# Optimization experiments

Measured on AMD Instinct MI355X. Metric: run time of the kernel, lower is better.

Reference implementation:

```python
import math
import jax, jax.numpy as jnp
import numpy as np
from jax import lax

INPUT_SIZE = 736
PATCH_SIZE = 16
PATCH_LENGTH = 768
EMBED_DIM = 768
BATCH = 32
N_RINGS = INPUT_SIZE // 2  # 368 rings, equal_interval=1


def _precompute_gather(input_size=INPUT_SIZE, patch_length=PATCH_LENGTH):
    """Replicates the torch buffer construction: per-radius-ring pixel masks
    sorted by angle, fused with the per-ring linear (align_corners=True)
    resize to patch_length. Returns flat gather indices and lerp weights."""
    H = W = input_size
    yc = np.arange(H) - (H - 1) / 2.0
    xc = np.arange(W) - (W - 1) / 2.0
    yy, xx = np.meshgrid(yc, xc, indexing='ij')  # yy=row offset, xx=col offset
    radius = np.sqrt(xx ** 2 + yy ** 2)
    R = input_size // 2
    off = (W - 1) / 2.0
    j = np.arange(patch_length)
    idx0_all, idx1_all, w_all = [], [], []
    for low in range(R):
        high = low + 1
        m = (radius > low) & (radius <= high)
        ry, rx = np.nonzero(m)  # row-major order, same as torch .nonzero()
        # Faithful to torch quirk: unbind names (x, y) = (row-off, col-off)
        xv = ry - off
        yv = rx - off
        deg = np.arctan2(-yv, xv) * 180.0 / math.pi
        flat = ry * W + rx
        order = np.argsort(deg, kind='stable')
        flat = flat[order]
        L = len(flat)
        # F.interpolate(mode='linear', align_corners=True) to patch_length
        if L == 1:
            src = np.zeros(patch_length)
        else:
            src = j * (L - 1) / (patch_length - 1)
        i0 = np.clip(np.floor(src).astype(np.int64), 0, L - 1)
        i1 = np.minimum(i0 + 1, L - 1)
        wt = (src - i0).astype(np.float32)
        idx0_all.append(flat[i0])
        idx1_all.append(flat[i1])
        w_all.append(wt)
    idx0 = np.concatenate(idx0_all).astype(np.int32)
    idx1 = np.concatenate(idx1_all).astype(np.int32)
    w = np.concatenate(w_all).astype(np.float32)
    return idx0, idx1, w


def setup_inputs() -> dict:
    key = jax.random.key(0)
    k1, k2 = jax.random.split(key)
    x = jax.random.normal(k1, (BATCH, 3, INPUT_SIZE, INPUT_SIZE), dtype=jnp.float32)
    fan_in = 3 * PATCH_SIZE * PATCH_SIZE
    conv_w = jax.random.normal(k2, (EMBED_DIM, 3, PATCH_SIZE, PATCH_SIZE), dtype=jnp.float32) / np.sqrt(fan_in)
    conv_b = jnp.zeros((EMBED_DIM,), dtype=jnp.float32)
    idx0, idx1, w = _precompute_gather()
    return {
        'x': x,
        'conv_w': conv_w,
        'conv_b': conv_b,
        'idx0': jnp.asarray(idx0),
        'idx1': jnp.asarray(idx1),
        'w': jnp.asarray(w),
    }


def reference(x, conv_w, conv_b, idx0, idx1, w):
    N = x.shape[0]
    flat = x.reshape(N, 3, -1)  # [N, 3, H*W]
    # Fused irregular gather + per-ring linear resize (lerp between neighbors)
    g0 = flat[:, :, idx0]
    g1 = flat[:, :, idx1]
    patches = g0 * (1.0 - w) + g1 * w  # [N, 3, N_RINGS*PATCH_LENGTH]
    patches = patches.reshape(N, 3, N_RINGS, PATCH_LENGTH)  # [N,3,368,768]
    out = lax.conv_general_dilated(
        patches, conv_w,
        window_strides=(PATCH_SIZE, PATCH_SIZE),
        padding='VALID',
        dimension_numbers=('NCHW', 'OIHW', 'NCHW'),
    )
    return out + conv_b[None, :, None, None]  # [N, 768, 23, 48]
```

## Files before the change

kernel.cpp:

```cpp
#include <hip/hip_runtime.h>
#include <hip/hip_bf16.h>
#include <stdint.h>

#define INPUT_SIZE   736
#define PLANE_ELEMS  (736*736)
#define N_RINGS      368
#define PATCH_LEN    768
#define EMBED        768
#define BATCH        32
#define KDIM         768
#define M_TOTAL      (BATCH*23*48)
#define P_PER_BATCH  1104
#define OUT_BATCH_STRIDE 847872
#define GATHER_T     (N_RINGS*PATCH_LEN)

typedef __bf16 bf16x8 __attribute__((ext_vector_type(8)));
typedef float  floatx4 __attribute__((ext_vector_type(4)));

static __device__ __forceinline__ unsigned short bf16bits(float f) {
    __hip_bfloat16 h = __float2bfloat16(f);
    return *reinterpret_cast<unsigned short*>(&h);
}

__global__ void wcast_kernel(const float* __restrict__ wsrc,
                             __hip_bfloat16* __restrict__ Wb) {
    int i = blockIdx.x * 256 + threadIdx.x;
    Wb[i] = __float2bfloat16(wsrc[i]);
}

__global__ void pack_kernel(const int*   __restrict__ idx0,
                            const int*   __restrict__ idx1,
                            const float* __restrict__ w,
                            int2* __restrict__ P) {
    int t = blockIdx.x * 256 + threadIdx.x;
    int i0 = idx0[t];
    int d  = idx1[t] - i0;
    unsigned w16 = (unsigned)(w[t] * 65536.0f);
    if (w16 > 65535u) w16 = 65535u;
    P[t] = make_int2(i0, (int)((w16 << 16) | ((unsigned)d & 0xFFFFu)));
}

__global__ void gather_kernel(const float* __restrict__ x,
                              const int2*  __restrict__ P,
                              __hip_bfloat16* __restrict__ A) {
    int b    = blockIdx.x;
    int half = b & 1;
    int bb   = b >> 1;
    int band = bb % 23;
    int nc   = bb / 23;
    int c    = nc % 3;
    int n    = nc / 3;
    const float* plane = x + (size_t)nc * PLANE_ELEMS;

    int wv   = threadIdx.x >> 6;
    int lane = threadIdx.x & 63;
    int rr   = lane >> 2;
    int ps   = lane & 3;
    int aw   = wv >> 1;
    int hb   = wv & 1;
    int r    = band * 16 + rr;

    int tbase = r * PATCH_LEN + half * 384 + aw * 16 + hb * 8 + ps * 2;
    int k     = c * 256 + rr * 16 + hb * 8 + ps * 2;
    size_t mbase = (size_t)(n * P_PER_BATCH + band * 48 + half * 24 + aw);
    __hip_bfloat16* aptr = A + mbase * KDIM + k;

    #pragma unroll 4
    for (int it = 0; it < 12; it++) {
        int4 q = *reinterpret_cast<const int4*>(&P[tbase + it * 32]);
        int   i0a = q.x;
        int   i1a = i0a + (int)(short)((unsigned)q.y & 0xFFFFu);
        float wa  = (float)((unsigned)q.y >> 16) * (1.0f / 65536.0f);
        float va  = plane[i0a] * (1.0f - wa) + plane[i1a] * wa;
        int   i0b = q.z;
        int   i1b = i0b + (int)(short)((unsigned)q.w & 0xFFFFu);
        float wb  = (float)((unsigned)q.w >> 16) * (1.0f / 65536.0f);
        float vb  = plane[i0b] * (1.0f - wb) + plane[i1b] * wb;
        *reinterpret_cast<ushort2*>(aptr + (size_t)(it * 2) * KDIM) =
            make_ushort2(bf16bits(va), bf16bits(vb));
    }
}

__global__ __launch_bounds__(256) void gemm_kernel(
        const __hip_bfloat16* __restrict__ A,
        const __hip_bfloat16* __restrict__ Wb,
        const float* __restrict__ cb,
        float* __restrict__ out)
{
    __shared__ __hip_bfloat16 As[128 * 32];
    __shared__ __hip_bfloat16 Bs[128 * 32];

    const int tid  = threadIdx.x;
    const int lane = tid & 63;
    const int wv   = tid >> 6;
    const int wm   = wv & 1;
    const int wn   = wv >> 1;
    const int quad = lane >> 4;
    const int l16  = lane & 15;

    const int bn = blockIdx.x;
    const int bm = blockIdx.y;

    floatx4 acc[4][4];
    #pragma unroll
    for (int i = 0; i < 4; i++)
        #pragma unroll
        for (int j = 0; j < 4; j++)
            acc[i][j] = (floatx4){0.f, 0.f, 0.f, 0.f};

    const int srow = tid >> 2;
    const int kofs = (tid & 3) * 8;
    const __hip_bfloat16* aSrc = A  + (size_t)(bm * 128 + srow) * KDIM + kofs;
    const __hip_bfloat16* bSrc = Wb + (size_t)(bn * 128 + srow) * KDIM + kofs;
    __hip_bfloat16* aDst = As + tid * 8;
    __hip_bfloat16* bDst = Bs + tid * 8;

    for (int kt = 0; kt < 24; kt++) {
        const __hip_bfloat16* ap = aSrc + kt * 32;
        const __hip_bfloat16* bp = bSrc + kt * 32;
        __builtin_amdgcn_global_load_lds(
            (const __attribute__((address_space(1))) void*)(const void*)ap,
            (__attribute__((address_space(3))) void*)(void*)aDst, 16, 0, 0);
        __builtin_amdgcn_global_load_lds(
            (const __attribute__((address_space(1))) void*)(const void*)(ap + (size_t)64 * KDIM),
            (__attribute__((address_space(3))) void*)(void*)(aDst + 64 * 32), 16, 0, 0);
        __builtin_amdgcn_global_load_lds(
            (const __attribute__((address_space(1))) void*)(const void*)bp,
            (__attribute__((address_space(3))) void*)(void*)bDst, 16, 0, 0);
        __builtin_amdgcn_global_load_lds(
            (const __attribute__((address_space(1))) void*)(const void*)(bp + (size_t)64 * KDIM),
            (__attribute__((address_space(3))) void*)(void*)(bDst + 64 * 32), 16, 0, 0);
        __syncthreads();

        bf16x8 af[4], bfr[4];
        #pragma unroll
        for (int mi = 0; mi < 4; mi++) {
            int ml = wm * 64 + mi * 16 + l16;
            af[mi] = *(const bf16x8*)(As + ml * 32 + quad * 8);
        }
        #pragma unroll
        for (int ni = 0; ni < 4; ni++) {
            int el = wn * 64 + ni * 16 + l16;
            bfr[ni] = *(const bf16x8*)(Bs + el * 32 + quad * 8);
        }
        #pragma unroll
        for (int mi = 0; mi < 4; mi++)
            #pragma unroll
            for (int ni = 0; ni < 4; ni++)
                acc[mi][ni] = __builtin_amdgcn_mfma_f32_16x16x32_bf16(
                                  af[mi], bfr[ni], acc[mi][ni], 0, 0, 0);
        __syncthreads();
    }

    const int m0 = bm * 128 + wm * 64;
    const int e0 = bn * 128 + wn * 64;
    #pragma unroll
    for (int ni = 0; ni < 4; ni++) {
        int eg = e0 + ni * 16 + l16;
        float bias = cb[eg];
        #pragma unroll
        for (int mi = 0; mi < 4; mi++) {
            int mg = m0 + mi * 16 + quad * 4;
            int nb = mg / P_PER_BATCH;
            int p  = mg - nb * P_PER_BATCH;
            floatx4 v = acc[mi][ni];
            v[0] += bias; v[1] += bias; v[2] += bias; v[3] += bias;
            *(floatx4*)(out + (size_t)nb * OUT_BATCH_STRIDE
                            + (size_t)eg * P_PER_BATCH + p) = v;
        }
    }
}

extern "C" void kernel_launch(void* const* d_in, const int* in_sizes, int n_in,
                              void* d_out, int out_size, void* d_ws, size_t ws_size,
                              hipStream_t stream) {
    const float* x      = (const float*)d_in[0];
    const float* conv_w = (const float*)d_in[1];
    const float* conv_b = (const float*)d_in[2];
    const int*   idx0   = (const int*)  d_in[3];
    const int*   idx1   = (const int*)  d_in[4];
    const float* w      = (const float*)d_in[5];
    float* out = (float*)d_out;

    __hip_bfloat16* A  = (__hip_bfloat16*)d_ws;
    __hip_bfloat16* Wb = A + (size_t)M_TOTAL * KDIM;
    int2*           P  = (int2*)(Wb + (size_t)EMBED * KDIM);

    wcast_kernel<<<dim3(EMBED * KDIM / 256), dim3(256), 0, stream>>>(conv_w, Wb);

    pack_kernel<<<dim3(GATHER_T / 256), dim3(256), 0, stream>>>(idx0, idx1, w, P);

    gather_kernel<<<dim3(BATCH * 3 * (N_RINGS / 16) * 2), dim3(256), 0, stream>>>(
        x, P, A);

    gemm_kernel<<<dim3(EMBED / 128, M_TOTAL / 128), dim3(256), 0, stream>>>(
        A, Wb, conv_b, out);
}
```

Before: 440.7 us.

## Rewrite GEMM with 256x128 tiles, multi-stage LDS pipeline and swizzled layout

Result: slower. 450.3 us (+2.2%).

```diff
diff --git a/kernel.cpp b/kernel.cpp
--- a/kernel.cpp
+++ b/kernel.cpp
@@ -21,6 +21,12 @@
     __hip_bfloat16 h = __float2bfloat16(f);
     return *reinterpret_cast<unsigned short*>(&h);
 }
+
+#define GLDS(gptr, lptr) __builtin_amdgcn_global_load_lds( \
+    (const __attribute__((address_space(1))) void*)(const void*)(gptr), \
+    (__attribute__((address_space(3))) void*)(void*)(lptr), 16, 0, 0)
+#define FENCE() asm volatile("" ::: "memory")
+#define BAR()   do { FENCE(); __builtin_amdgcn_s_barrier(); FENCE(); } while (0)
 
 __global__ void wcast_kernel(const float* __restrict__ wsrc,
                              __hip_bfloat16* __restrict__ Wb) {
@@ -81,20 +87,20 @@
     }
 }
 
-__global__ __launch_bounds__(256) void gemm_kernel(
-        const __hip_bfloat16* __restrict__ A,
+__global__ __launch_bounds__(512) void gemm_kernel(
+        const __hip_bfloat16* __restrict__ Ap,
         const __hip_bfloat16* __restrict__ Wb,
         const float* __restrict__ cb,
         float* __restrict__ out)
 {
-    __shared__ __hip_bfloat16 As[128 * 32];
-    __shared__ __hip_bfloat16 Bs[128 * 32];
+    __shared__ __hip_bfloat16 As[3 * 256 * 64];
+    __shared__ __hip_bfloat16 Bs[2 * 128 * 64];
 
     const int tid  = threadIdx.x;
     const int lane = tid & 63;
     const int wv   = tid >> 6;
-    const int wm   = wv & 1;
-    const int wn   = wv >> 1;
+    const int wm   = wv >> 1;
+    const int wn   = wv & 1;
     const int quad = lane >> 4;
     const int l16  = lane & 15;
 
@@ -108,51 +114,110 @@
         for (int j = 0; j < 4; j++)
             acc[i][j] = (floatx4){0.f, 0.f, 0.f, 0.f};
 
-    const int srow = tid >> 2;
-    const int kofs = (tid & 3) * 8;
-    const __hip_bfloat16* aSrc = A  + (size_t)(bm * 128 + srow) * KDIM + kofs;
-    const __hip_bfloat16* bSrc = Wb + (size_t)(bn * 128 + srow) * KDIM + kofs;
-    __hip_bfloat16* aDst = As + tid * 8;
-    __hip_bfloat16* bDst = Bs + tid * 8;
-
-    for (int kt = 0; kt < 24; kt++) {
-        const __hip_bfloat16* ap = aSrc + kt * 32;
-        const __hip_bfloat16* bp = bSrc + kt * 32;
-        __builtin_amdgcn_global_load_lds(
-            (const __attribute__((address_space(1))) void*)(const void*)ap,
-            (__attribute__((address_space(3))) void*)(void*)aDst, 16, 0, 0);
-        __builtin_amdgcn_global_load_lds(
-            (const __attribute__((address_space(1))) void*)(const void*)(ap + (size_t)64 * KDIM),
-            (__attribute__((address_space(3))) void*)(void*)(aDst + 64 * 32), 16, 0, 0);
-        __builtin_amdgcn_global_load_lds(
-            (const __attribute__((address_space(1))) void*)(const void*)bp,
-            (__attribute__((address_space(3))) void*)(void*)bDst, 16, 0, 0);
-        __builtin_amdgcn_global_load_lds(
-            (const __attribute__((address_space(1))) void*)(const void*)(bp + (size_t)64 * KDIM),
-            (__attribute__((address_space(3))) void*)(void*)(bDst + 64 * 32), 16, 0, 0);
-        __syncthreads();
-
-        bf16x8 af[4], bfr[4];
-        #pragma unroll
-        for (int mi = 0; mi < 4; mi++) {
-            int ml = wm * 64 + mi * 16 + l16;
-            af[mi] = *(const bf16x8*)(As + ml * 32 + quad * 8);
+    const __hip_bfloat16* aG[4]; __hip_bfloat16* aL[4];
+    #pragma unroll
+    for (int l = 0; l < 4; l++) {
+        int u   = l * 512 + tid;
+        int row = u >> 3;
+        int col = ((u & 7) ^ (row & 7)) * 8;
+        aG[l] = Ap + (size_t)(bm * 256 + row) * KDIM + col;
+        aL[l] = As + u * 8;
+    }
+    const __hip_bfloat16* bG[2]; __hip_bfloat16* bL[2];
+    #pragma unroll
+    for (int l = 0; l < 2; l++) {
+        int u   = l * 512 + tid;
+        int row = u >> 3;
+        int col = ((u & 7) ^ (row & 7)) * 8;
+        bG[l] = Wb + (size_t)(bn * 128 + row) * KDIM + col;
+        bL[l] = Bs + u * 8;
+    }
+
+    #pragma unroll
+    for (int l = 0; l < 4; l++) GLDS(aG[l], aL[l]);
+    #pragma unroll
+    for (int l = 0; l < 2; l++) GLDS(bG[l], bL[l]);
+    #pragma unroll
+    for (int l = 0; l < 4; l++) GLDS(aG[l] + 64, aL[l] + 16384);
+    asm volatile("s_waitcnt vmcnt(4)" ::: "memory");
+    BAR();
+
+    bf16x8 afr[2][2], bfr[4][2];
+
+    for (int kt = 0; kt < 12; kt++) {
+        const int sA  = kt % 3;
+        const int sB  = kt & 1;
+        const int sA2 = (kt + 2) % 3;
+        const int sB1 = (kt + 1) & 1;
+        const __hip_bfloat16* asl = As + sA * 16384;
+        const __hip_bfloat16* bsl = Bs + sB * 8192;
+
+        #pragma unroll
+        for (int mi = 0; mi < 2; mi++) {
+            int r = wm * 64 + mi * 16 + l16;
+            #pragma unroll
+            for (int kk = 0; kk < 2; kk++) {
+                int sl = (kk * 4 + quad) ^ (r & 7);
+                afr[mi][kk] = *(const bf16x8*)(asl + r * 64 + sl * 8);
+            }
         }
         #pragma unroll
         for (int ni = 0; ni < 4; ni++) {
-            int el = wn * 64 + ni * 16 + l16;
-            bfr[ni] = *(const bf16x8*)(Bs + el * 32 + quad * 8);
-        }
-        #pragma unroll
-        for (int mi = 0; mi < 4; mi++)
-            #pragma unroll
-            for (int ni = 0; ni < 4; ni++)
-                acc[mi][ni] = __builtin_amdgcn_mfma_f32_16x16x32_bf16(
-                                  af[mi], bfr[ni], acc[mi][ni], 0, 0, 0);
-        __syncthreads();
-    }
-
-    const int m0 = bm * 128 + wm * 64;
+            int r = wn * 64 + ni * 16 + l16;
+            #pragma unroll
+            for (int kk = 0; kk < 2; kk++) {
+                int sl = (kk * 4 + quad) ^ (r & 7);
+                bfr[ni][kk] = *(const bf16x8*)(bsl + r * 64 + sl * 8);
+            }
+        }
+        GLDS(bG[0] + (kt + 1) * 64, bL[0] + sB1 * 8192);
+        GLDS(bG[1] + (kt + 1) * 64, bL[1] + sB1 * 8192);
+        GLDS(aG[0] + (kt + 2) * 64, aL[0] + sA2 * 16384);
+        BAR();
+        __builtin_amdgcn_sched_barrier(0);
+        __builtin_amdgcn_s_setprio(1);
+        #pragma unroll
+        for (int ni = 0; ni < 4; ni++)
+            #pragma unroll
+            for (int kk = 0; kk < 2; kk++) {
+                acc[0][ni] = __builtin_amdgcn_mfma_f32_16x16x32_bf16(
+                                 afr[0][kk], bfr[ni][kk], acc[0][ni], 0, 0, 0);
+                acc[1][ni] = __builtin_amdgcn_mfma_f32_16x16x32_bf16(
+                                 afr[1][kk], bfr[ni][kk], acc[1][ni], 0, 0, 0);
+            }
+        __builtin_amdgcn_s_setprio(0);
+        BAR();
+
+        #pragma unroll
+        for (int mi = 0; mi < 2; mi++) {
+            int r = wm * 64 + (mi + 2) * 16 + l16;
+            #pragma unroll
+            for (int kk = 0; kk < 2; kk++) {
+                int sl = (kk * 4 + quad) ^ (r & 7);
+                afr[mi][kk] = *(const bf16x8*)(asl + r * 64 + sl * 8);
+            }
+        }
+        GLDS(aG[1] + (kt + 2) * 64, aL[1] + sA2 * 16384);
+        GLDS(aG[2] + (kt + 2) * 64, aL[2] + sA2 * 16384);
+        GLDS(aG[3] + (kt + 2) * 64, aL[3] + sA2 * 16384);
+        BAR();
+        __builtin_amdgcn_sched_barrier(0);
+        __builtin_amdgcn_s_setprio(1);
+        #pragma unroll
+        for (int ni = 0; ni < 4; ni++)
+            #pragma unroll
+            for (int kk = 0; kk < 2; kk++) {
+                acc[2][ni] = __builtin_amdgcn_mfma_f32_16x16x32_bf16(
+                                 afr[0][kk], bfr[ni][kk], acc[2][ni], 0, 0, 0);
+                acc[3][ni] = __builtin_amdgcn_mfma_f32_16x16x32_bf16(
+                                 afr[1][kk], bfr[ni][kk], acc[3][ni], 0, 0, 0);
+            }
+        __builtin_amdgcn_s_setprio(0);
+        asm volatile("s_waitcnt vmcnt(4)" ::: "memory");
+        BAR();
+    }
+
+    const int m0 = bm * 256 + wm * 64;
     const int e0 = bn * 128 + wn * 64;
     #pragma unroll
     for (int ni = 0; ni < 4; ni++) {
@@ -193,6 +258,6 @@
     gather_kernel<<<dim3(BATCH * 3 * (N_RINGS / 16) * 2), dim3(256), 0, stream>>>(
         x, P, A);
 
-    gemm_kernel<<<dim3(EMBED / 128, M_TOTAL / 128), dim3(256), 0, stream>>>(
+    gemm_kernel<<<dim3(EMBED / 128, M_TOTAL / 256), dim3(512), 0, stream>>>(
         A, Wb, conv_b, out);
 }
```
